# Performance work log

Hardware: AMD Instinct MI355X
Metric: run time of the kernel (lower is better)

The kernel has to match this reference:

```python
import jax, jax.numpy as jnp
import numpy as np
import math

EPS = jnp.float32(1.1920929e-07)      # torch.finfo(torch.float).eps
FMIN = jnp.finfo(jnp.float32).min     # torch.finfo(torch.float).min
NEG = jnp.float32(-1e9)


def setup_inputs() -> dict:
    key = jax.random.key(0)
    ks = jax.random.split(key, 9)
    bs, l, sub, tgt, hidden, t_vocab, voc = 16, 1024, 2, 256, 512, 2000, 3000
    return {
        "out_logits": jax.random.normal(ks[0], (bs, tgt, t_vocab), jnp.float32),
        "feature": jax.random.normal(ks[1], (bs, tgt, hidden), jnp.float32),
        "memory_raw": jax.random.normal(ks[2], (bs, l, hidden), jnp.float32),
        "content_e": jax.random.randint(ks[3], (bs, l * sub), 0, voc, jnp.int64
                                        if jax.config.jax_enable_x64 else jnp.int32),
        "Wq": jax.random.normal(ks[4], (hidden, hidden), jnp.float32) * 0.02,
        "bq": jax.random.normal(ks[5], (hidden,), jnp.float32) * 0.02,
        "Wk": jax.random.normal(ks[6], (hidden, hidden * sub), jnp.float32) * 0.02,
        "bk": jax.random.normal(ks[7], (hidden * sub,), jnp.float32) * 0.02,
        "sentinel": jax.random.uniform(ks[8], (1, hidden), jnp.float32),
        "voc_len": 3000,
    }


def reference(out_logits, feature, memory_raw, content_e, Wq, bq, Wk, bk, sentinel, voc_len):
    bs, l, hidden = memory_raw.shape
    tgt_len = feature.shape[1]
    subtokens = Wk.shape[1] // hidden
    src_len = l * subtokens

    # decode(): out = log_softmax(prob(feature)); key_linear + subtoken expansion
    out = jax.nn.log_softmax(out_logits, axis=-1)                     # (bs, t, t_vocab)
    memory = (memory_raw @ Wk + bk).reshape(bs, src_len, hidden)      # (bs, s, h)
    key_padding_mask = content_e == 0                                 # (bs, s)

    # pointer(): attention over memory + sentinel
    pointer_key = jnp.concatenate(
        [memory, jnp.broadcast_to(sentinel[None, :, :], (bs, 1, hidden))], axis=1)
    pointer_query = jax.nn.gelu(feature @ Wq + bq, approximate=False) # (bs, t, h)
    atten = jnp.einsum('bth,bsh->bts', pointer_query, pointer_key) / math.sqrt(hidden)

    mask = jnp.concatenate(
        [key_padding_mask, jnp.zeros((bs, 1), bool)], axis=-1)[:, None, :]
    atten = jnp.where(mask, NEG, atten)
    atten = jax.nn.log_softmax(atten, axis=-1)                        # (bs, t, s+1)

    pointer_gate = atten[:, :, -1:]                                   # (bs, t, 1)
    exp_atten = jnp.exp(atten[:, :, :-1])                             # (bs, t, s)

    # scatter-add over src positions by extended-vocab id (== one-hot M einsum)
    def scat(ea_b, ce_b):  # ea_b: (t, s)  ce_b: (s,)
        return jax.ops.segment_sum(ea_b.T, ce_b, num_segments=voc_len).T  # (t, voc)
    pointer_atten_p = jax.vmap(scat)(exp_atten, content_e)            # (bs, t, voc)

    pointer_atten_log = jnp.log(pointer_atten_p + EPS)
    pointer_atten_log = pointer_atten_log - jnp.log1p(-jnp.exp(pointer_gate) + EPS)
    pointer_atten_log = jnp.where(jnp.isneginf(pointer_atten_log), FMIN, pointer_atten_log)

    pad = jnp.full((bs, tgt_len, voc_len - out.shape[-1]), -jnp.inf, jnp.float32)
    out = jnp.concatenate([out, pad], axis=-1)                        # (bs, t, voc)

    p = jnp.stack([out + pointer_gate,
                   pointer_atten_log + jnp.log(1.0 - jnp.exp(pointer_gate) + EPS)],
                  axis=-2)                                            # (bs, t, 2, voc)
    return jax.scipy.special.logsumexp(p, axis=-2)                    # (bs, t, voc)
```

## Files before the change

kernel.cpp:

```cpp
#include <hip/hip_runtime.h>
#include <math.h>

#define BSZ   16
#define LSEQ  1024
#define TGT   256
#define HID   512
#define TV    2000
#define VOC   3000
#define SRC   2048
#define NKE   1280
#define JOFF  640
#define SCALE 0.044194173824159216f

typedef unsigned short u16;
typedef __attribute__((ext_vector_type(8))) short bf16x8;
typedef __attribute__((ext_vector_type(4))) float f32x4;

__device__ __forceinline__ u16 f2bf(float x) {
    unsigned u = __float_as_uint(x);
    u += 0x7FFFu + ((u >> 16) & 1u);
    return (u16)(u >> 16);
}
__device__ __forceinline__ float bf2f(u16 x) {
    return __uint_as_float((unsigned)x << 16);
}

static __device__ __forceinline__ float gelu_exact(float x) {
    return 0.5f * x * (1.0f + erff(x * 0.70710678118654752f));
}

__device__ __forceinline__ void gload16(const u16* g, u16* l) {
    __builtin_amdgcn_global_load_lds(
        (const __attribute__((address_space(1))) unsigned int*)g,
        (__attribute__((address_space(3))) unsigned int*)l,
        16, 0, 0);
}

__device__ __forceinline__ void cast8_body(const float4* __restrict__ in,
                                           int4* __restrict__ out, int i) {
    float4 x = in[2 * i], y = in[2 * i + 1];
    unsigned p0 = (unsigned)f2bf(x.x) | ((unsigned)f2bf(x.y) << 16);
    unsigned p1 = (unsigned)f2bf(x.z) | ((unsigned)f2bf(x.w) << 16);
    unsigned p2 = (unsigned)f2bf(y.x) | ((unsigned)f2bf(y.y) << 16);
    unsigned p3 = (unsigned)f2bf(y.z) | ((unsigned)f2bf(y.w) << 16);
    out[i] = make_int4(p0, p1, p2, p3);
}

__global__ __launch_bounds__(256) void prep_a(
    const float* __restrict__ feature, const float* __restrict__ Wq,
    const float* __restrict__ Wk, const float* __restrict__ sentinel,
    const float* __restrict__ bk,
    int4* __restrict__ featb, u16* __restrict__ wqT, u16* __restrict__ wkE,
    float* __restrict__ rowsum)
{
    __shared__ float t[32][33];
    const int id = blockIdx.x;
    const int tid = threadIdx.x;
    if (id < 1024) {
        cast8_body((const float4*)feature, featb, id * 256 + tid);
    } else if (id < 1280) {
        int id2 = id - 1024;
        int bx = (id2 & 15) * 32, by = (id2 >> 4) * 32;
        const int tx = tid & 31, ty = tid >> 5;
        #pragma unroll
        for (int k = 0; k < 4; ++k)
            t[ty + 8 * k][tx] = Wq[(size_t)(by + ty + 8 * k) * 512 + bx + tx];
        __syncthreads();
        #pragma unroll
        for (int k = 0; k < 4; ++k)
            wqT[(size_t)(bx + ty + 8 * k) * 512 + by + tx] = f2bf(t[tx][ty + 8 * k]);
    } else if (id < 1600) {
        const int rr = (id - 1280) * 4 + (tid >> 6);
        const int c = (tid & 63) * 8;
        const int j = rr >= JOFF;
        const int dd = rr - j * JOFF;
        u16* dst = wkE + (size_t)rr * HID + c;
        if (dd < 512) {
            const float* src = Wk + (size_t)dd * 1024 + j * 512 + c;
            #pragma unroll
            for (int k = 0; k < 8; ++k) dst[k] = f2bf(src[k]);
        } else if (dd == 512) {
            #pragma unroll
            for (int k = 0; k < 8; ++k) dst[k] = f2bf(sentinel[c + k]);
        } else if (dd == 513) {
            #pragma unroll
            for (int k = 0; k < 8; ++k) dst[k] = f2bf(bk[j * 512 + c + k]);
        } else {
            #pragma unroll
            for (int k = 0; k < 8; ++k) dst[k] = 0;
        }
    } else {
        float4* rz = (float4*)rowsum;
        for (int i = tid; i < 1024; i += 256) rz[i] = make_float4(0.f, 0.f, 0.f, 0.f);
    }
}

__global__ __launch_bounds__(256) void k_query(
    const u16* __restrict__ feat, const u16* __restrict__ wqT,
    const float* __restrict__ bq, u16* __restrict__ queryb,
    const float* __restrict__ memory_raw, int4* __restrict__ memb)
{
    __shared__ u16 sbuf[2 * 2048 * 2];
    const int id = blockIdx.x;
    const int tid = threadIdx.x;
    if (id >= 512) {
        cast8_body((const float4*)memory_raw, memb, (id - 512) * 256 + tid);
        return;
    }
    u16* As = sbuf;
    u16* Bs = sbuf + 2 * 2048;
    const int lane = tid & 63;
    const int w = tid >> 6;
    const int wr = (w >> 1) * 32, wc = (w & 1) * 32;
    const int m0 = (id >> 3) * 64, n0 = (id & 7) * 64;

    const int srow = tid >> 2, scol = (tid & 3) * 8;
    const u16* gA = feat + (size_t)(m0 + srow) * HID + scol;
    const u16* gB = wqT + (size_t)(n0 + srow) * HID + scol;

    const int la = lane & 15, lb = lane >> 4;
    f32x4 acc[2][2] = {};

    gload16(gA, As + w * 512);
    gload16(gB, Bs + w * 512);

    int cur = 0;
    for (int k0 = 0; k0 < HID; k0 += 32) {
        __syncthreads();
        const u16* Asb = As + cur * 2048;
        const u16* Bsb = Bs + cur * 2048;
        bf16x8 af[2], bf[2];
        #pragma unroll
        for (int i = 0; i < 2; ++i)
            af[i] = *(const bf16x8*)(Asb + (wr + i * 16 + la) * 32 + lb * 8);
        #pragma unroll
        for (int j = 0; j < 2; ++j)
            bf[j] = *(const bf16x8*)(Bsb + (wc + j * 16 + la) * 32 + lb * 8);
        if (k0 + 32 < HID) {
            const int nb = cur ^ 1;
            gload16(gA + k0 + 32, As + nb * 2048 + w * 512);
            gload16(gB + k0 + 32, Bs + nb * 2048 + w * 512);
        }
        #pragma unroll
        for (int i = 0; i < 2; ++i)
            #pragma unroll
            for (int j = 0; j < 2; ++j)
                acc[i][j] = __builtin_amdgcn_mfma_f32_16x16x32_bf16(af[i], bf[j], acc[i][j], 0, 0, 0);
        cur ^= 1;
    }

    const int r_l = (lane >> 4) * 4, c_l = lane & 15;
    #pragma unroll
    for (int j = 0; j < 2; ++j) {
        const int n = n0 + wc + j * 16 + c_l;
        const float bv = bq[n];
        #pragma unroll
        for (int i = 0; i < 2; ++i)
            #pragma unroll
            for (int r = 0; r < 4; ++r) {
                const int m = m0 + wr + i * 16 + r_l + r;
                queryb[(size_t)m * HID + n] = f2bf(gelu_exact(acc[i][j][r] + bv));
            }
    }
}

template<int EPI, int LDA, int LDB>
__device__ __forceinline__ void gemm_body(
    int m0, int n0, int z,
    const u16* __restrict__ Abase, const u16* __restrict__ Bbase,
    u16* __restrict__ outb,
    const int* __restrict__ ce, float* __restrict__ rowsum,
    u16* __restrict__ As, u16* __restrict__ Bs)
{
    const int tid = threadIdx.x;
    const int lane = tid & 63;
    const int w = tid >> 6;
    const int wr = (w >> 1) * 64, wc = (w & 1) * 64;

    const u16* Ag = Abase;
    const u16* Bg = Bbase;
    if (EPI == 2) {
        Ag = Abase + (size_t)(z >> 1) * LSEQ * HID;
        Bg = Bbase + (size_t)(z >> 1) * TGT * NKE + (size_t)(z & 1) * JOFF;
    }

    const int chunkrow = lane >> 2;
    const int colc = (lane & 3) * 8;
    const int c0 = w * 2, c1 = c0 + 1;
    const u16* gA0 = Ag + (size_t)(m0 + c0 * 16 + chunkrow) * LDA + colc;
    const u16* gA1 = Ag + (size_t)(m0 + c1 * 16 + chunkrow) * LDA + colc;
    const u16* gB0 = Bg + (size_t)(n0 + c0 * 16 + chunkrow) * LDB + colc;
    const u16* gB1 = Bg + (size_t)(n0 + c1 * 16 + chunkrow) * LDB + colc;

    const int la = lane & 15, lb = lane >> 4;
    f32x4 acc[4][4] = {};

    gload16(gA0, As + c0 * 512);
    gload16(gA1, As + c1 * 512);
    gload16(gB0, Bs + c0 * 512);
    gload16(gB1, Bs + c1 * 512);

    int cur = 0;
    for (int k0 = 0; k0 < HID; k0 += 32) {
        __syncthreads();
        const u16* Asb = As + cur * 4096;
        const u16* Bsb = Bs + cur * 4096;
        bf16x8 af[4], bfv[4];
        #pragma unroll
        for (int i = 0; i < 4; ++i)
            af[i] = *(const bf16x8*)(Asb + (wr + i * 16 + la) * 32 + lb * 8);
        #pragma unroll
        for (int j = 0; j < 4; ++j)
            bfv[j] = *(const bf16x8*)(Bsb + (wc + j * 16 + la) * 32 + lb * 8);
        if (k0 + 32 < HID) {
            const int nb = cur ^ 1;
            u16* An = As + nb * 4096;
            u16* Bn = Bs + nb * 4096;
            gload16(gA0 + k0 + 32, An + c0 * 512);
            gload16(gA1 + k0 + 32, An + c1 * 512);
            gload16(gB0 + k0 + 32, Bn + c0 * 512);
            gload16(gB1 + k0 + 32, Bn + c1 * 512);
        }
        #pragma unroll
        for (int i = 0; i < 4; ++i)
            #pragma unroll
            for (int j = 0; j < 4; ++j)
                acc[i][j] = __builtin_amdgcn_mfma_f32_16x16x32_bf16(af[i], bfv[j], acc[i][j], 0, 0, 0);
        cur ^= 1;
    }

    const int r_l = (lane >> 4) * 4, c_l = lane & 15;
    if (EPI == 3) {
        #pragma unroll
        for (int j = 0; j < 4; ++j) {
            const int n = n0 + wc + j * 16 + c_l;
            #pragma unroll
            for (int i = 0; i < 4; ++i)
                #pragma unroll
                for (int r = 0; r < 4; ++r) {
                    const int m = m0 + wr + i * 16 + r_l + r;
                    outb[(size_t)m * NKE + n] = f2bf(acc[i][j][r]);
                }
        }
    } else {
        const int b = z >> 1, jj = z & 1;
        float biasc[4];
        #pragma unroll
        for (int j = 0; j < 4; ++j) {
            const int n = n0 + wc + j * 16 + c_l;
            biasc[j] = bf2f(Bbase[(size_t)(b * TGT + n) * NKE + jj * JOFF + 513]);
        }
        const int* ceb = ce + (size_t)b * SRC;
        float csum[4] = {0.f, 0.f, 0.f, 0.f};
        #pragma unroll
        for (int i = 0; i < 4; ++i)
            #pragma unroll
            for (int r = 0; r < 4; ++r) {
                const int m = m0 + wr + i * 16 + r_l + r;
                const int cm = ceb[2 * m + jj];
                const size_t rowbase = ((size_t)b * SRC + jj * 1024 + m) * TGT;
                #pragma unroll
                for (int j = 0; j < 4; ++j) {
                    float ev = (cm == 0) ? 0.f
                             : __expf((acc[i][j][r] + biasc[j]) * SCALE);
                    outb[rowbase + n0 + wc + j * 16 + c_l] = f2bf(ev);
                    csum[j] += ev;
                }
            }
        #pragma unroll
        for (int j = 0; j < 4; ++j) {
            csum[j] += __shfl_xor(csum[j], 16, 64);
            csum[j] += __shfl_xor(csum[j], 32, 64);
        }
        const int jsel = lane >> 4;
        float myv = (jsel == 0) ? csum[0] : (jsel == 1) ? csum[1]
                  : (jsel == 2) ? csum[2] : csum[3];
        atomicAdd(&rowsum[b * TGT + n0 + wc + jsel * 16 + c_l], myv);
    }
}

__global__ __launch_bounds__(256) void k_qk(
    const u16* __restrict__ queryb, const u16* __restrict__ wkE,
    u16* __restrict__ qkb,
    const float* __restrict__ logits, float* __restrict__ lse,
    const int* __restrict__ ce, int* __restrict__ boff, u16* __restrict__ bucket)
{
    __shared__ u16 sbuf[4 * 4096];
    const int id = blockIdx.x;
    const int tid = threadIdx.x;
    if (id < 320) {
        gemm_body<3, 512, 512>((id / 10) * 128, (id % 10) * 128, 0,
                               queryb, wkE, qkb, nullptr, nullptr,
                               sbuf, sbuf + 2 * 4096);
    } else if (id < 1344) {
        const int row = (id - 320) * 4 + (tid >> 6);
        const int lane = tid & 63;
        const float4* lrow4 = (const float4*)(logits + (size_t)row * TV);
        float4 v4[8];
        float m = -INFINITY;
        #pragma unroll
        for (int k = 0; k < 8; ++k) {
            int idx = lane + 64 * k;
            if (idx < 500) {
                v4[k] = lrow4[idx];
                m = fmaxf(m, fmaxf(fmaxf(v4[k].x, v4[k].y), fmaxf(v4[k].z, v4[k].w)));
            } else {
                v4[k] = make_float4(-INFINITY, -INFINITY, -INFINITY, -INFINITY);
            }
        }
        #pragma unroll
        for (int o = 32; o > 0; o >>= 1) m = fmaxf(m, __shfl_xor(m, o, 64));
        float s = 0.f;
        #pragma unroll
        for (int k = 0; k < 8; ++k)
            s += __expf(v4[k].x - m) + __expf(v4[k].y - m)
               + __expf(v4[k].z - m) + __expf(v4[k].w - m);
        #pragma unroll
        for (int o = 32; o > 0; o >>= 1) s += __shfl_xor(s, o, 64);
        if (lane == 0) lse[row] = m + __logf(s);
    } else {
        const int b = id - 1344;
        int* cnt = (int*)sbuf;
        int* part = cnt + VOC;
        const int* ceb = ce + (size_t)b * SRC;
        for (int v = tid; v < VOC; v += 256) cnt[v] = 0;
        __syncthreads();
        for (int s = tid; s < SRC; s += 256) atomicAdd(&cnt[ceb[s]], 1);
        __syncthreads();
        const int base = tid * 12;
        int lc[12];
        int tot = 0;
        #pragma unroll
        for (int k = 0; k < 12; ++k) {
            int v = base + k;
            lc[k] = (v < VOC) ? cnt[v] : 0;
            tot += lc[k];
        }
        part[tid] = tot;
        __syncthreads();
        for (int d = 1; d < 256; d <<= 1) {
            int val = (tid >= d) ? part[tid - d] : 0;
            __syncthreads();
            part[tid] += val;
            __syncthreads();
        }
        int run = part[tid] - tot;
        int* boffb = boff + b * 3008;
        #pragma unroll
        for (int k = 0; k < 12; ++k) {
            int v = base + k;
            if (v < VOC) { boffb[v] = run; cnt[v] = run; run += lc[k]; }
        }
        if (tid == 0) boffb[VOC] = SRC;
        __syncthreads();
        for (int s = tid; s < SRC; s += 256) {
            int idv = ceb[s];
            int jl = (s & 1) * 1024 + (s >> 1);
            int pos = atomicAdd(&cnt[idv], 1);
            bucket[(size_t)b * SRC + pos] = (u16)jl;
        }
    }
}

__global__ __launch_bounds__(256) void gemm_atten(
    const u16* __restrict__ memb, const u16* __restrict__ qkb,
    const int* __restrict__ ce, float* __restrict__ rowsum,
    u16* __restrict__ etb)
{
    __shared__ u16 As[2 * 4096];
    __shared__ u16 Bs[2 * 4096];
    const int i = blockIdx.x;
    const int xcd = i & 7, slot = i >> 3;
    const int bjj = xcd + 8 * (slot >> 4);
    const int inner = slot & 15;
    gemm_body<2, 512, NKE>((inner >> 1) * 128, (inner & 1) * 128, bjj,
                           memb, qkb, etb, ce, rowsum, As, Bs);
}

__global__ __launch_bounds__(256) void combine(
    const u16* __restrict__ etb, const u16* __restrict__ bucket,
    const int* __restrict__ boff, const u16* __restrict__ qkb,
    const float* __restrict__ rowsum, const float* __restrict__ lse,
    const float* __restrict__ out_logits, float* __restrict__ out)
{
    __shared__ float acc[8][256];
    __shared__ u16 sbuck[SRC];
    __shared__ float rcInv[8], rcGZ[8], rcEdl[8], rcDl[8];
    const int i = blockIdx.x;
    const int xcd = i & 7, slot = i >> 3;
    const int b = xcd + 8 * (slot / 384);
    const int inner = slot % 384;
    const int tc = inner / 12, vs = inner % 12;
    const int t0 = tc * 8;
    const int vbase = vs * 256;
    const int tid = threadIdx.x;
    const float EPSF = 1.1920929e-07f;

    if (tid < 8) {
        const int bt = b * TGT + t0 + tid;
        const float sent_v = bf2f(qkb[(size_t)bt * NKE + 512]) * SCALE;
        const float se = __expf(sent_v);
        const float sm = rowsum[bt] + se;
        const float inv = 1.0f / sm;
        const float g = sent_v - __logf(sm);
        const float eg = se * inv;
        const float dl = __logf(1.0f - eg + EPSF) - log1pf(-eg + EPSF);
        rcInv[tid] = inv;
        rcGZ[tid] = g - lse[bt];
        rcEdl[tid] = __expf(dl);
        rcDl[tid] = dl;
    }

    const int* boffb = boff + b * 3008;
    const u16* bukb = bucket + (size_t)b * SRC;
    const u16* etbb = etb + (size_t)b * SRC * TGT;

    const int vend = (vbase + 256 < VOC) ? vbase + 256 : VOC;
    const int e_lo = boffb[vbase];
    const int e_hi = boffb[vend];
    for (int e = e_lo + tid; e < e_hi; e += 256) sbuck[e - e_lo] = bukb[e];
    __syncthreads();

    {
        float a[8] = {0.f, 0.f, 0.f, 0.f, 0.f, 0.f, 0.f, 0.f};
        const int v = vbase + tid;
        if (v < VOC) {
            const int i0 = boffb[v] - e_lo;
            const int i1 = boffb[v + 1] - e_lo;
            for (int e = i0; e < i1; ++e) {
                const int s = sbuck[e];
                int4 u = *(const int4*)(etbb + (size_t)s * TGT + t0);
                a[0] += bf2f((u16)(u.x & 0xffff));
                a[1] += bf2f((u16)((unsigned)u.x >> 16));
                a[2] += bf2f((u16)(u.y & 0xffff));
                a[3] += bf2f((u16)((unsigned)u.y >> 16));
                a[4] += bf2f((u16)(u.z & 0xffff));
                a[5] += bf2f((u16)((unsigned)u.z >> 16));
                a[6] += bf2f((u16)(u.w & 0xffff));
                a[7] += bf2f((u16)((unsigned)u.w >> 16));
            }
        }
        #pragma unroll
        for (int k = 0; k < 8; ++k) acc[k][tid] = a[k];
    }
    __syncthreads();

    const int r = tid >> 5;
    const int vl0 = tid & 31;
    const int bt = b * TGT + t0 + r;
    const float inv = rcInv[r], gZ = rcGZ[r], edl = rcEdl[r], dlv = rcDl[r];
    const float* lrow = out_logits + (size_t)bt * TV;
    float* orow = out + (size_t)bt * VOC;
    #pragma unroll
    for (int kk = 0; kk < 8; ++kk) {
        const int vloc = vl0 + 32 * kk;
        const int v = vbase + vloc;
        if (v >= VOC) continue;
        float pv = acc[r][vloc] * inv + EPSF;
        float o;
        if (v < TV) o = __logf(__expf(lrow[v] + gZ) + pv * edl);
        else        o = __logf(pv) + dlv;
        orow[v] = o;
    }
}

extern "C" void kernel_launch(void* const* d_in, const int* in_sizes, int n_in,
                              void* d_out, int out_size, void* d_ws, size_t ws_size,
                              hipStream_t stream) {
    const float* out_logits = (const float*)d_in[0];
    const float* feature    = (const float*)d_in[1];
    const float* memory_raw = (const float*)d_in[2];
    const int*   content_e  = (const int*)d_in[3];
    const float* Wq = (const float*)d_in[4];
    const float* bq = (const float*)d_in[5];
    const float* Wk = (const float*)d_in[6];
    const float* bk = (const float*)d_in[7];
    const float* sentinel = (const float*)d_in[8];
    float* out = (float*)d_out;

    u16* memb   = (u16*)d_ws;
    u16* featb  = memb   + (size_t)16384 * 512;
    u16* wqT    = featb  + (size_t)4096 * 512;
    u16* wkE    = wqT    + (size_t)512 * 512;
    u16* queryb = wkE    + (size_t)NKE * 512;
    u16* qkb    = queryb + (size_t)4096 * 512;
    u16* etb    = qkb    + (size_t)4096 * NKE;
    float* rowsum = (float*)(etb + (size_t)BSZ * SRC * TGT);
    float* lse   = rowsum + 4096;
    int* boff = (int*)(lse + 4096);
    u16* bucket = (u16*)(boff + 16 * 3008);

    prep_a<<<1601, 256, 0, stream>>>(feature, Wq, Wk, sentinel, bk,
                                     (int4*)featb, wqT, wkE, rowsum);
    k_query<<<4608, 256, 0, stream>>>(featb, wqT, bq, queryb, memory_raw, (int4*)memb);
    k_qk<<<1360, 256, 0, stream>>>(queryb, wkE, qkb, out_logits, lse,
                                   content_e, boff, bucket);
    gemm_atten<<<512, 256, 0, stream>>>(memb, qkb, content_e, rowsum, etb);
    combine<<<6144, 256, 0, stream>>>(etb, bucket, boff, qkb,
                                      rowsum, lse, out_logits, out);
}
```

Measured before the change: 93.32 us.

## Parallelize combine over bucket entries with LDS atomics and wider vocab chunks

The combine kernel now splits work by source entries instead of vocab ids. Each thread takes bucket entries, which now pack the vocab id together with the source index, and adds the 8 attention values into shared-memory accumulators with atomics. This removes the load imbalance of per-vocab serial loops, where a thread owning a frequent id iterated many times while most threads idled. Vocab chunks double to 512, which halves the grid and the redundant per-block setup, at the cost of LDS atomic contention and a larger shared-memory footprint.

```diff
diff --git a/kernel.cpp b/kernel.cpp
--- a/kernel.cpp
+++ b/kernel.cpp
@@ -10,9 +10,11 @@
 #define SRC   2048
 #define NKE   1280
 #define JOFF  640
+#define VCH   512
 #define SCALE 0.044194173824159216f
 
 typedef unsigned short u16;
+typedef unsigned int u32;
 typedef __attribute__((ext_vector_type(8))) short bf16x8;
 typedef __attribute__((ext_vector_type(4))) float f32x4;
 
@@ -283,7 +285,7 @@
     const u16* __restrict__ queryb, const u16* __restrict__ wkE,
     u16* __restrict__ qkb,
     const float* __restrict__ logits, float* __restrict__ lse,
-    const int* __restrict__ ce, int* __restrict__ boff, u16* __restrict__ bucket)
+    const int* __restrict__ ce, int* __restrict__ boff, u32* __restrict__ bucket)
 {
     __shared__ u16 sbuf[4 * 4096];
     const int id = blockIdx.x;
@@ -357,7 +359,7 @@
             int idv = ceb[s];
             int jl = (s & 1) * 1024 + (s >> 1);
             int pos = atomicAdd(&cnt[idv], 1);
-            bucket[(size_t)b * SRC + pos] = (u16)jl;
+            bucket[(size_t)b * SRC + pos] = ((u32)idv << 11) | (u32)jl;
         }
     }
 }
@@ -378,21 +380,21 @@
 }
 
 __global__ __launch_bounds__(256) void combine(
-    const u16* __restrict__ etb, const u16* __restrict__ bucket,
+    const u16* __restrict__ etb, const u32* __restrict__ bucket,
     const int* __restrict__ boff, const u16* __restrict__ qkb,
     const float* __restrict__ rowsum, const float* __restrict__ lse,
     const float* __restrict__ out_logits, float* __restrict__ out)
 {
-    __shared__ float acc[8][256];
-    __shared__ u16 sbuck[SRC];
+    __shared__ float acc[8][VCH];
+    __shared__ u32 sbuck[SRC];
     __shared__ float rcInv[8], rcGZ[8], rcEdl[8], rcDl[8];
     const int i = blockIdx.x;
     const int xcd = i & 7, slot = i >> 3;
-    const int b = xcd + 8 * (slot / 384);
-    const int inner = slot % 384;
-    const int tc = inner / 12, vs = inner % 12;
+    const int b = xcd + 8 * (slot / 192);
+    const int inner = slot % 192;
+    const int tc = inner / 6, vs = inner % 6;
     const int t0 = tc * 8;
-    const int vbase = vs * 256;
+    const int vbase = vs * VCH;
     const int tid = threadIdx.x;
     const float EPSF = 1.1920929e-07f;
 
@@ -412,36 +414,33 @@
     }
 
     const int* boffb = boff + b * 3008;
-    const u16* bukb = bucket + (size_t)b * SRC;
+    const u32* bukb = bucket + (size_t)b * SRC;
     const u16* etbb = etb + (size_t)b * SRC * TGT;
 
-    const int vend = (vbase + 256 < VOC) ? vbase + 256 : VOC;
+    const int vend = (vbase + VCH < VOC) ? vbase + VCH : VOC;
     const int e_lo = boffb[vbase];
-    const int e_hi = boffb[vend];
-    for (int e = e_lo + tid; e < e_hi; e += 256) sbuck[e - e_lo] = bukb[e];
+    const int cnt = boffb[vend] - e_lo;
+    for (int e = tid; e < cnt; e += 256) sbuck[e] = bukb[e_lo + e];
+    #pragma unroll
+    for (int k = 0; k < 8; ++k) {
+        acc[k][tid] = 0.f;
+        acc[k][tid + 256] = 0.f;
+    }
     __syncthreads();
 
-    {
-        float a[8] = {0.f, 0.f, 0.f, 0.f, 0.f, 0.f, 0.f, 0.f};
-        const int v = vbase + tid;
-        if (v < VOC) {
-            const int i0 = boffb[v] - e_lo;
-            const int i1 = boffb[v + 1] - e_lo;
-            for (int e = i0; e < i1; ++e) {
-                const int s = sbuck[e];
-                int4 u = *(const int4*)(etbb + (size_t)s * TGT + t0);
-                a[0] += bf2f((u16)(u.x & 0xffff));
-                a[1] += bf2f((u16)((unsigned)u.x >> 16));
-                a[2] += bf2f((u16)(u.y & 0xffff));
-                a[3] += bf2f((u16)((unsigned)u.y >> 16));
-                a[4] += bf2f((u16)(u.z & 0xffff));
-                a[5] += bf2f((u16)((unsigned)u.z >> 16));
-                a[6] += bf2f((u16)(u.w & 0xffff));
-                a[7] += bf2f((u16)((unsigned)u.w >> 16));
-            }
-        }
-        #pragma unroll
-        for (int k = 0; k < 8; ++k) acc[k][tid] = a[k];
+    for (int e = tid; e < cnt; e += 256) {
+        const u32 pk = sbuck[e];
+        const int vloc = (int)(pk >> 11) - vbase;
+        const int s = (int)(pk & 2047u);
+        int4 u = *(const int4*)(etbb + (size_t)s * TGT + t0);
+        atomicAdd(&acc[0][vloc], bf2f((u16)(u.x & 0xffff)));
+        atomicAdd(&acc[1][vloc], bf2f((u16)((unsigned)u.x >> 16)));
+        atomicAdd(&acc[2][vloc], bf2f((u16)(u.y & 0xffff)));
+        atomicAdd(&acc[3][vloc], bf2f((u16)((unsigned)u.y >> 16)));
+        atomicAdd(&acc[4][vloc], bf2f((u16)(u.z & 0xffff)));
+        atomicAdd(&acc[5][vloc], bf2f((u16)((unsigned)u.z >> 16)));
+        atomicAdd(&acc[6][vloc], bf2f((u16)(u.w & 0xffff)));
+        atomicAdd(&acc[7][vloc], bf2f((u16)((unsigned)u.w >> 16)));
     }
     __syncthreads();
 
@@ -452,7 +451,7 @@
     const float* lrow = out_logits + (size_t)bt * TV;
     float* orow = out + (size_t)bt * VOC;
     #pragma unroll
-    for (int kk = 0; kk < 8; ++kk) {
+    for (int kk = 0; kk < 16; ++kk) {
         const int vloc = vl0 + 32 * kk;
         const int v = vbase + vloc;
         if (v >= VOC) continue;
@@ -488,7 +487,7 @@
     float* rowsum = (float*)(etb + (size_t)BSZ * SRC * TGT);
     float* lse   = rowsum + 4096;
     int* boff = (int*)(lse + 4096);
-    u16* bucket = (u16*)(boff + 16 * 3008);
+    u32* bucket = (u32*)(boff + 16 * 3008);
 
     prep_a<<<1601, 256, 0, stream>>>(feature, Wq, Wk, sentinel, bk,
                                      (int4*)featb, wqT, wkE, rowsum);
@@ -496,6 +495,6 @@
     k_qk<<<1360, 256, 0, stream>>>(queryb, wkE, qkb, out_logits, lse,
                                    content_e, boff, bucket);
     gemm_atten<<<512, 256, 0, stream>>>(memb, qkb, content_e, rowsum, etb);
-    combine<<<6144, 256, 0, stream>>>(etb, bucket, boff, qkb,
+    combine<<<3072, 256, 0, stream>>>(etb, bucket, boff, qkb,
                                       rowsum, lse, out_logits, out);
 }
```

New measurement: 130.2 us. 1.39x slower.
